# Optimization experiments

Measured on AMD Instinct MI355X. Metric: run time of the kernel, lower is better.

The kernel has to match this reference:

```python
import jax, jax.numpy as jnp
import numpy as np

EPS = 1e-5

def _linear(x, w, b):
    # torch nn.Linear convention: w is [out, in]
    return jnp.einsum('...i,oi->...o', x, w) + b

def _l2_normalize(x, axis=-1):
    n = jnp.sqrt(jnp.sum(x * x, axis=axis, keepdims=True))
    return x / jnp.maximum(n, 1e-12)

def _online_softmax_scan(sim):
    # sim: [B, H, L]. Running max m_t and running sum s_t = sum_{i<=t} exp(sim_i - m_t)
    def combine(a, b):
        ma, sa = a
        mb, sb = b
        m = jnp.maximum(ma, mb)
        s = sa * jnp.exp(ma - m) + sb * jnp.exp(mb - m)
        return m, s
    m_scan, s_scan = jax.lax.associative_scan(combine, (sim, jnp.ones_like(sim)), axis=2)
    return m_scan, s_scan


def setup_inputs() -> dict:
    key = jax.random.key(0)
    ks = jax.random.split(key, 8)
    B, L, D = 2, 2048, 256
    H, h = 8, 32
    s = 1.0 / np.sqrt(D)
    inp = {
        'x': jax.random.normal(ks[0], (B, L, D), jnp.float32),
        'wq_w': jax.random.normal(ks[1], (D, D), jnp.float32) * s,
        'wq_b': jnp.zeros((D,), jnp.float32),
        'wk_w': jax.random.normal(ks[2], (D, D), jnp.float32) * s,
        'wk_b': jnp.zeros((D,), jnp.float32),
        'wv_w': jax.random.normal(ks[3], (D, D), jnp.float32) * s,
        'wv_b': jnp.zeros((D,), jnp.float32),
        'wo_w': jax.random.normal(ks[4], (D, D), jnp.float32) * s,
        'wo_b': jnp.zeros((D,), jnp.float32),
        'wg_w': jax.random.normal(ks[5], (1, h * h), jnp.float32) * (1.0 / np.sqrt(h * h)),
        'wg_b': jnp.zeros((1,), jnp.float32),
        'kv_norm_scale': jnp.ones((1, H, 1, h, h), jnp.float32),
        'qk_norm_scale': jnp.full((1, H, 1), 1.0 / np.sqrt(h), jnp.float32),
    }
    return inp


def reference(x, wq_w, wq_b, wk_w, wk_b, wv_w, wv_b, wo_w, wo_b,
              wg_w, wg_b, kv_norm_scale, qk_norm_scale):
    B, L, D = x.shape
    H, h = kv_norm_scale.shape[1], kv_norm_scale.shape[3]

    q = _linear(x, wq_w, wq_b).reshape(B, L, H, h).transpose(0, 2, 1, 3)  # bhld
    k = _linear(x, wk_w, wk_b).reshape(B, L, H, h).transpose(0, 2, 1, 3)
    v = _linear(x, wv_w, wv_b).reshape(B, L, H, h).transpose(0, 2, 1, 3)

    sim = jnp.einsum('bhld,bhld->bhl', q, k) * qk_norm_scale  # [B,H,L]

    k = _l2_normalize(k)
    v = _l2_normalize(v)

    # outer-product KV state per position: [B,H,L,h,h]
    Z = jnp.einsum('bhld,bhle->bhlde', v, k) * kv_norm_scale

    # gating: squared ReLU of linear over flattened h*h features
    gate_inputs = Z.reshape(B, H, L, h * h)
    gates_logits = jnp.einsum('bhli,oi->bhlo', gate_inputs, wg_w) + wg_b  # [B,H,L,1]
    gates = jnp.square(jax.nn.relu(gates_logits)) + EPS
    gates = gates[..., None]  # [B,H,L,1,1]
    gated_Z = gates * Z

    # associative scans along L
    m_scan, s_scan = _online_softmax_scan(sim)        # [B,H,L]
    Z_scan = jnp.cumsum(gated_Z, axis=2)              # [B,H,L,h,h]
    g_scan = jnp.cumsum(gates, axis=2)                # [B,H,L,1,1]

    softmax_weights = (jnp.exp(sim - m_scan) / (s_scan + EPS))[..., None, None]
    gated_weights = Z_scan / (g_scan + EPS)
    attn_weights = gated_weights * (1.0 + jax.nn.silu(softmax_weights))

    ctxt = jnp.einsum('bhld,bhlde->bhle', q, attn_weights)
    ctxt = ctxt.transpose(0, 2, 1, 3).reshape(B, L, D)
    return _linear(ctxt, wo_w, wo_b)
```

## Files before the change

### kernel.cpp

```cpp
#include <hip/hip_runtime.h>
#include <math.h>

#define EPSV 1e-5f

static constexpr int Ls = 2048, Hh = 8;
static constexpr int NCH = 64, T = 32;

typedef unsigned short u16;
using frag  = __attribute__((ext_vector_type(8))) short;
using f32x4 = __attribute__((ext_vector_type(4))) float;

__device__ __forceinline__ void split_bf16(float v, u16& hi, u16& lo) {
    const unsigned u = __float_as_uint(v);
    hi = (u16)(u >> 16);
    const float hf = __uint_as_float((unsigned)hi << 16);
    lo = (u16)(__float_as_uint(v - hf) >> 16);
}

__device__ __forceinline__ unsigned pk2(u16 a, u16 b) {
    return (unsigned)a | ((unsigned)b << 16);
}

__device__ __forceinline__ void split8(const float4& a, const float4& b,
                                       uint4& hi, uint4& lo) {
    u16 h[8], l[8];
    const float f[8] = {a.x, a.y, a.z, a.w, b.x, b.y, b.z, b.w};
#pragma unroll
    for (int i = 0; i < 8; ++i) split_bf16(f[i], h[i], l[i]);
    hi = make_uint4(pk2(h[0], h[1]), pk2(h[2], h[3]), pk2(h[4], h[5]), pk2(h[6], h[7]));
    lo = make_uint4(pk2(l[0], l[1]), pk2(l[2], l[3]), pk2(l[4], l[5]), pk2(l[6], l[7]));
}

__global__ __launch_bounds__(256) void qkv_fused(
    const float* __restrict__ x,
    const float* __restrict__ wq, const float* __restrict__ wk, const float* __restrict__ wv,
    const float* __restrict__ bq, const float* __restrict__ bk, const float* __restrict__ bv,
    const float* __restrict__ wg_w, const float* __restrict__ wg_b,
    const float* __restrict__ kvs, const float* __restrict__ qks,
    float* __restrict__ qh, float* __restrict__ kh, float* __restrict__ vh,
    float* __restrict__ simG, float* __restrict__ gG,
    float* __restrict__ ZcT, float* __restrict__ mT, float* __restrict__ sT,
    float* __restrict__ gTt)
{
    constexpr int LDK = 40;
    constexpr int LDT = 68;
    __shared__ __align__(16) float smemf[3 * 64 * LDT];
    __shared__ __align__(16) float wkT[2][32 * 36];
    __shared__ float lsim[2][64], lg2[2][64];

    u16* As_hi = (u16*)smemf;
    u16* As_lo = As_hi + 2560;
    u16* Wst   = As_lo + 2560;
    float* Qt = smemf;
    float* Kt = Qt + 64 * LDT;
    float* Vt = Kt + 64 * LDT;

    const int tid = threadIdx.x;
    const int mt = blockIdx.x, nt = blockIdx.y;
    const int m0 = mt * 64, ncol0 = nt * 64;
    const int bidx = m0 >> 11, lg = m0 & (Ls - 1);
    const int wave = tid >> 6, lane = tid & 63;
    const int l15 = lane & 15, quad = lane >> 4;
    const int srow = tid >> 2, sk = (tid & 3) * 8;

    for (int i = tid; i < 2048; i += 256) {
        const int h = i >> 10, de = i & 1023;
        const int d = de >> 5, e = de & 31;
        wkT[h][e * 36 + d] = wg_w[de] * kvs[(nt * 2 + h) * 1024 + de];
    }

    const float* Wsrc[3] = {wq, wk, wv};
    f32x4 acc[3][4] = {};

    for (int k0 = 0; k0 < 256; k0 += 32) {
        const float4 a0 = *(const float4*)&x[(size_t)(m0 + srow) * 256 + k0 + sk];
        const float4 a1 = *(const float4*)&x[(size_t)(m0 + srow) * 256 + k0 + sk + 4];
        float4 w0[3], w1[3];
#pragma unroll
        for (int w = 0; w < 3; ++w) {
            w0[w] = *(const float4*)&Wsrc[w][(size_t)(ncol0 + srow) * 256 + k0 + sk];
            w1[w] = *(const float4*)&Wsrc[w][(size_t)(ncol0 + srow) * 256 + k0 + sk + 4];
        }
        __syncthreads();
        {
            uint4 hi, lo;
            split8(a0, a1, hi, lo);
            *(uint4*)&As_hi[srow * LDK + sk] = hi;
            *(uint4*)&As_lo[srow * LDK + sk] = lo;
#pragma unroll
            for (int w = 0; w < 3; ++w) {
                split8(w0[w], w1[w], hi, lo);
                *(uint4*)&Wst[w * 5120 + srow * LDK + sk] = hi;
                *(uint4*)&Wst[w * 5120 + 2560 + srow * LDK + sk] = lo;
            }
        }
        __syncthreads();

        const frag ah = *(const frag*)&As_hi[(wave * 16 + l15) * LDK + quad * 8];
        const frag al = *(const frag*)&As_lo[(wave * 16 + l15) * LDK + quad * 8];
#pragma unroll
        for (int w = 0; w < 3; ++w)
#pragma unroll
            for (int cf = 0; cf < 4; ++cf) {
                const u16* bp = &Wst[w * 5120 + (cf * 16 + l15) * LDK + quad * 8];
                const frag bh = *(const frag*)bp;
                const frag bl = *(const frag*)(bp + 2560);
                acc[w][cf] = __builtin_amdgcn_mfma_f32_16x16x32_bf16(ah, bh, acc[w][cf], 0, 0, 0);
                acc[w][cf] = __builtin_amdgcn_mfma_f32_16x16x32_bf16(ah, bl, acc[w][cf], 0, 0, 0);
                acc[w][cf] = __builtin_amdgcn_mfma_f32_16x16x32_bf16(al, bh, acc[w][cf], 0, 0, 0);
            }
    }
    __syncthreads();

    {
        float* tiles[3] = {Qt, Kt, Vt};
        const float* biases[3] = {bq, bk, bv};
#pragma unroll
        for (int w = 0; w < 3; ++w)
#pragma unroll
            for (int cf = 0; cf < 4; ++cf) {
                const int col = cf * 16 + l15;
                const float bias = biases[w][ncol0 + col];
#pragma unroll
                for (int r = 0; r < 4; ++r) {
                    const int m = wave * 16 + quad * 4 + r;
                    tiles[w][m * LDT + col] = acc[w][cf][r] + bias;
                }
            }
    }
    __syncthreads();

    if (tid < 128) {
        const int h = tid >> 6, l = tid & 63;
        const int rb = l * LDT + h * 32;
        float4 kr[8], vr[8];
        float ksum = 0.f, vsum = 0.f, qk = 0.f;
#pragma unroll
        for (int e4 = 0; e4 < 8; ++e4) {
            kr[e4] = *(const float4*)&Kt[rb + e4 * 4];
            vr[e4] = *(const float4*)&Vt[rb + e4 * 4];
            const float4 q4 = *(const float4*)&Qt[rb + e4 * 4];
            ksum += kr[e4].x * kr[e4].x + kr[e4].y * kr[e4].y + kr[e4].z * kr[e4].z + kr[e4].w * kr[e4].w;
            vsum += vr[e4].x * vr[e4].x + vr[e4].y * vr[e4].y + vr[e4].z * vr[e4].z + vr[e4].w * vr[e4].w;
            qk   += q4.x * kr[e4].x + q4.y * kr[e4].y + q4.z * kr[e4].z + q4.w * kr[e4].w;
        }
        const float kscale = 1.f / fmaxf(sqrtf(ksum), 1e-12f);
        const float vscale = 1.f / fmaxf(sqrtf(vsum), 1e-12f);
#pragma unroll
        for (int e4 = 0; e4 < 8; ++e4) {
            float4 k4 = kr[e4], v4 = vr[e4];
            k4.x *= kscale; k4.y *= kscale; k4.z *= kscale; k4.w *= kscale;
            v4.x *= vscale; v4.y *= vscale; v4.z *= vscale; v4.w *= vscale;
            *(float4*)&Kt[rb + e4 * 4] = k4;
            *(float4*)&Vt[rb + e4 * 4] = v4;
        }
        const float sim = qk * qks[nt * 2 + h];
        lsim[h][l] = sim;
        simG[(size_t)(bidx * 8 + nt * 2 + h) * Ls + lg + l] = sim;
    }
    __syncthreads();

    {
        const float* tl[3] = {Qt, Kt, Vt};
        float* gl[3] = {qh, kh, vh};
#pragma unroll
        for (int arr = 0; arr < 3; ++arr)
#pragma unroll
            for (int it = 0; it < 4; ++it) {
                const int idx = it * 1024 + tid * 4;
                const int h = idx >> 11, rem = idx & 2047;
                const int l = rem >> 5, e4 = rem & 31;
                const float4 v = *(const float4*)&tl[arr][l * LDT + h * 32 + e4];
                *(float4*)&gl[arr][(size_t)(bidx * 8 + nt * 2 + h) * 65536 +
                                   (size_t)(lg + l) * 32 + e4] = v;
            }
    }

    {
        const int task = tid >> 1, half = tid & 1;
        const int h = task >> 6, l = task & 63;
        float4 vr[8];
#pragma unroll
        for (int d4 = 0; d4 < 8; ++d4)
            vr[d4] = *(const float4*)&Vt[l * LDT + h * 32 + d4 * 4];
        float u = 0.f;
        const int e0 = half * 16;
#pragma unroll 4
        for (int e = e0; e < e0 + 16; ++e) {
            float4 s4 = make_float4(0.f, 0.f, 0.f, 0.f);
#pragma unroll
            for (int d4 = 0; d4 < 8; ++d4) {
                const float4 w4 = *(const float4*)&wkT[h][e * 36 + d4 * 4];
                s4.x = fmaf(vr[d4].x, w4.x, s4.x);
                s4.y = fmaf(vr[d4].y, w4.y, s4.y);
                s4.z = fmaf(vr[d4].z, w4.z, s4.z);
                s4.w = fmaf(vr[d4].w, w4.w, s4.w);
            }
            u = fmaf(s4.x + s4.y + s4.z + s4.w, Kt[l * LDT + h * 32 + e], u);
        }
        u += __shfl_xor(u, 1);
        if (half == 0) {
            const float r = fmaxf(u + wg_b[0], 0.f);
            const float g = r * r + EPSV;
            lg2[h][l] = g;
            gG[(size_t)(bidx * 8 + nt * 2 + h) * Ls + lg + l] = g;
        }
    }
    __syncthreads();

    {
        const int d = tid >> 3, e4m = (tid & 7) * 4;
#pragma unroll
        for (int h = 0; h < 2; ++h)
#pragma unroll
            for (int cc = 0; cc < 2; ++cc) {
                float4 z4 = make_float4(0.f, 0.f, 0.f, 0.f);
#pragma unroll 8
                for (int l = 0; l < 32; ++l) {
                    const int lr = cc * 32 + l;
                    const float gv = lg2[h][lr] * Vt[lr * LDT + h * 32 + d];
                    const float4 k4 = *(const float4*)&Kt[lr * LDT + h * 32 + e4m];
                    z4.x = fmaf(gv, k4.x, z4.x);
                    z4.y = fmaf(gv, k4.y, z4.y);
                    z4.z = fmaf(gv, k4.z, z4.z);
                    z4.w = fmaf(gv, k4.w, z4.w);
                }
                const int bhg = bidx * 8 + nt * 2 + h;
                const int cg = (lg >> 5) + cc;
                *(float4*)&ZcT[((size_t)bhg * NCH + cg) * 1024 + d * 32 + e4m] = z4;
            }
    }

    {
        const int h = wave >> 1, cc = wave & 1;
        if (lane < 32) {
            const int lr = cc * 32 + lane;
            float m = lsim[h][lr], s = 1.f, g = lg2[h][lr];
#pragma unroll
            for (int off = 16; off; off >>= 1) {
                const float mo = __shfl_xor(m, off);
                const float so = __shfl_xor(s, off);
                const float mn = fmaxf(m, mo);
                s = s * __expf(m - mn) + so * __expf(mo - mn);
                m = mn;
                g += __shfl_xor(g, off);
            }
            if (lane == 0) {
                const int bhg = bidx * 8 + nt * 2 + h;
                const int cg = (lg >> 5) + cc;
                mT[bhg * NCH + cg] = m;
                sT[bhg * NCH + cg] = s;
                gTt[bhg * NCH + cg] = g;
            }
        }
    }
}

__global__ __launch_bounds__(256) void prefix_kernel(
    float* __restrict__ Zc, float* __restrict__ mT, float* __restrict__ sT,
    float* __restrict__ gTt,
    const float* __restrict__ kvs, float* __restrict__ aW, float* __restrict__ bW,
    int* __restrict__ flagW)
{
    __shared__ float sc[64 * 64];
    const int bh = blockIdx.x, seg = blockIdx.y;
    const int tid = threadIdx.x;
    float* Zb = Zc + (size_t)bh * NCH * 1024 + seg * 64;

#pragma unroll
    for (int it = 0; it < 16; ++it) {
        const int idx = it * 256 + tid;
        const int cc = idx >> 6, e = idx & 63;
        sc[idx] = Zb[(size_t)cc * 1024 + e];
    }
    __syncthreads();
#pragma unroll
    for (int st = 1; st < 64; st <<= 1) {
        float tmp[16];
#pragma unroll
        for (int it = 0; it < 16; ++it) {
            const int idx = it * 256 + tid;
            tmp[it] = ((idx >> 6) >= st) ? sc[idx - st * 64] : 0.f;
        }
        __syncthreads();
#pragma unroll
        for (int it = 0; it < 16; ++it) sc[it * 256 + tid] += tmp[it];
        __syncthreads();
    }
#pragma unroll
    for (int it = 0; it < 16; ++it) {
        const int idx = it * 256 + tid;
        const int cc = idx >> 6, e = idx & 63;
        Zb[(size_t)cc * 1024 + e] = cc ? sc[idx - 64] : 0.f;
    }

    if (seg == 0 && tid < 64) {
        float m = mT[bh * NCH + tid], s = sT[bh * NCH + tid], g = gTt[bh * NCH + tid];
#pragma unroll
        for (int off = 1; off < 64; off <<= 1) {
            const float mo = __shfl_up(m, off);
            const float so = __shfl_up(s, off);
            const float go = __shfl_up(g, off);
            if (tid >= off) {
                const float mn = fmaxf(m, mo);
                s = s * __expf(m - mn) + so * __expf(mo - mn);
                m = mn;
                g += go;
            }
        }
        float me = __shfl_up(m, 1), se = __shfl_up(s, 1), ge = __shfl_up(g, 1);
        if (tid == 0) { me = -1e30f; se = 0.f; ge = 0.f; }
        mT[bh * NCH + tid] = me;
        sT[bh * NCH + tid] = se;
        gTt[bh * NCH + tid] = ge;
    }

    if (bh == 0 && seg == 1) {
        const int h = tid >> 5, e = tid & 31;
        const float* K = kvs + h * 1024;
        const float k00 = K[0];
        int ok = (k00 != 0.0f);
        for (int d = 0; d < 32; ++d) {
            const float lhs = K[d * 32 + e] * k00;
            const float rhs = K[d * 32] * K[e];
            const float diff = fabsf(lhs - rhs);
            if (diff > 1e-6f * fmaxf(fmaxf(fabsf(lhs), fabsf(rhs)), 1e-20f)) ok = 0;
        }
        aW[h * 32 + e] = K[e * 32];
        bW[h * 32 + e] = (k00 != 0.0f) ? K[e] / k00 : 0.f;
        const int allok = __syncthreads_and(ok);
        if (tid == 0) flagW[0] = allok;
    }
}

__global__ __launch_bounds__(256) void chunk_out_kernel(
    const float* __restrict__ qh, const float* __restrict__ knG, const float* __restrict__ vnG,
    const float* __restrict__ simG, const float* __restrict__ gG,
    const float* __restrict__ kvs,
    const float* __restrict__ ZcP, const float* __restrict__ mP,
    const float* __restrict__ sP, const float* __restrict__ gP,
    const float* __restrict__ aW, const float* __restrict__ bW,
    const int* __restrict__ flagW,
    u16* __restrict__ chi, u16* __restrict__ clo)
{
    __shared__ __align__(16) float qa[1024], knb[1024], zp[1024], sW[1024];
    __shared__ __align__(16) float vnT[32 * 36];
    __shared__ float lkvs[1024];
    __shared__ float lgS[32], lsimS[32], lwgt[32];
    const int tid = threadIdx.x;
    const int c = blockIdx.x, bh = blockIdx.y, h = bh & 7, b = bh >> 3;
    const int l = tid >> 3, e4 = (tid & 7) * 4;
    const size_t base4 = ((size_t)bh * Ls + (size_t)c * T) * 8 + tid;
    const int flag = flagW[0];

    const float4 qv4 = ((const float4*)qh)[base4];
    const float4 kn4 = ((const float4*)knG)[base4];
    const float4 vn4 = ((const float4*)vnG)[base4];
    const float4 z4  = ((const float4*)ZcP)[((size_t)bh * NCH + c) * 256 + tid];
    const float4 la4 = *(const float4*)&aW[h * 32 + e4];
    const float4 lb4 = *(const float4*)&bW[h * 32 + e4];
    if (tid < 32) {
        lgS[tid] = gG[bh * Ls + c * T + tid];
        lsimS[tid] = simG[bh * Ls + c * T + tid];
    }
    if (!flag) {
        *(float4*)&lkvs[tid * 4] = *(const float4*)&kvs[h * 1024 + tid * 4];
    }
    {
        float4 q = qv4, k = kn4;
        if (flag) {
            q.x *= la4.x; q.y *= la4.y; q.z *= la4.z; q.w *= la4.w;
            k.x *= lb4.x; k.y *= lb4.y; k.z *= lb4.z; k.w *= lb4.w;
        }
        *(float4*)&qa[l * 32 + e4] = q;
        *(float4*)&knb[l * 32 + e4] = k;
        *(float4*)&zp[tid * 4] = z4;
        vnT[(e4 + 0) * 36 + l] = vn4.x;
        vnT[(e4 + 1) * 36 + l] = vn4.y;
        vnT[(e4 + 2) * 36 + l] = vn4.z;
        vnT[(e4 + 3) * 36 + l] = vn4.w;
    }
    __syncthreads();

    if (tid < 32) {
        float m = lsimS[tid], s = 1.f, g = lgS[tid];
#pragma unroll
        for (int off = 1; off < 32; off <<= 1) {
            const float mo = __shfl_up(m, off);
            const float so = __shfl_up(s, off);
            const float go = __shfl_up(g, off);
            if (tid >= off) {
                const float mn = fmaxf(m, mo);
                s = s * __expf(m - mn) + so * __expf(mo - mn);
                m = mn;
                g += go;
            }
        }
        const float mp = mP[bh * NCH + c];
        const float sp = sP[bh * NCH + c];
        const float gp = gP[bh * NCH + c];
        const float mn = fmaxf(mp, m);
        s = sp * __expf(mp - mn) + s * __expf(m - mn);
        m = mn;
        g += gp;
        const float sw = __expf(lsimS[tid] - m) / (s + EPSV);
        const float sig = 1.f / (1.f + __expf(-sw));
        lwgt[tid] = (1.f + sw * sig) / (g + EPSV);
    }

    float4 y4 = make_float4(0.f, 0.f, 0.f, 0.f);
    if (flag) {
        float qrow[32];
#pragma unroll
        for (int d4 = 0; d4 < 8; ++d4)
            *(float4*)&qrow[d4 * 4] = *(const float4*)&qa[l * 32 + d4 * 4];
        float4 s4 = make_float4(0.f, 0.f, 0.f, 0.f);
#pragma unroll 8
        for (int d = 0; d < 32; ++d) {
            const float qd = qrow[d];
            const float4 v4 = *(const float4*)&vnT[d * 36 + e4];
            const float4 p4 = *(const float4*)&zp[d * 32 + e4];
            s4.x = fmaf(qd, v4.x, s4.x);
            s4.y = fmaf(qd, v4.y, s4.y);
            s4.z = fmaf(qd, v4.z, s4.z);
            s4.w = fmaf(qd, v4.w, s4.w);
            y4.x = fmaf(qd, p4.x, y4.x);
            y4.y = fmaf(qd, p4.y, y4.y);
            y4.z = fmaf(qd, p4.z, y4.z);
            y4.w = fmaf(qd, p4.w, y4.w);
        }
        y4.x *= lb4.x; y4.y *= lb4.y; y4.z *= lb4.z; y4.w *= lb4.w;
        const float4 lg4 = *(const float4*)&lgS[e4];
        float4 sm;
        sm.x = (e4 + 0 <= l) ? lg4.x * s4.x : 0.f;
        sm.y = (e4 + 1 <= l) ? lg4.y * s4.y : 0.f;
        sm.z = (e4 + 2 <= l) ? lg4.z * s4.z : 0.f;
        sm.w = (e4 + 3 <= l) ? lg4.w * s4.w : 0.f;
        *(float4*)&sW[l * 32 + e4] = sm;
        __syncthreads();
        float srow[32];
#pragma unroll
        for (int j4 = 0; j4 < 8; ++j4)
            *(float4*)&srow[j4 * 4] = *(const float4*)&sW[l * 32 + j4 * 4];
#pragma unroll 8
        for (int j = 0; j < 32; ++j) {
            const float sj = srow[j];
            const float4 k4 = *(const float4*)&knb[j * 32 + e4];
            y4.x = fmaf(sj, k4.x, y4.x);
            y4.y = fmaf(sj, k4.y, y4.y);
            y4.z = fmaf(sj, k4.z, y4.z);
            y4.w = fmaf(sj, k4.w, y4.w);
        }
    } else {
        __syncthreads();
        float* yp = &y4.x;
#pragma unroll
        for (int i = 0; i < 4; ++i) {
            const int e = e4 + i;
            float qe[32];
#pragma unroll
            for (int d = 0; d < 32; ++d)
                qe[d] = qa[l * 32 + d] * lkvs[d * 32 + e];
            float y = 0.f;
#pragma unroll
            for (int d = 0; d < 32; ++d)
                y = fmaf(qe[d], zp[d * 32 + e], y);
            for (int j = 0; j < 32; ++j) {
                float s = 0.f;
#pragma unroll
                for (int d = 0; d < 32; ++d)
                    s = fmaf(qe[d], vnT[d * 36 + j], s);
                if (j <= l) y = fmaf(lgS[j] * s, knb[j * 32 + e], y);
            }
            yp[i] = y;
        }
    }
    const float w = lwgt[l];
    ushort4 hi4, lo4;
    split_bf16(y4.x * w, hi4.x, lo4.x);
    split_bf16(y4.y * w, hi4.y, lo4.y);
    split_bf16(y4.z * w, hi4.z, lo4.z);
    split_bf16(y4.w * w, hi4.w, lo4.w);
    const size_t oidx = ((size_t)(b * Ls + c * T + l)) * 256 + h * 32 + e4;
    *(ushort4*)&chi[oidx] = hi4;
    *(ushort4*)&clo[oidx] = lo4;
}

__global__ __launch_bounds__(256) void out_gemm(
    const u16* __restrict__ Ahi, const u16* __restrict__ Alo,
    const float* __restrict__ wo, const float* __restrict__ bo,
    float* __restrict__ out)
{
    constexpr int LDK = 40;
    __shared__ __align__(16) u16 As_hi[64 * LDK];
    __shared__ __align__(16) u16 As_lo[64 * LDK];
    __shared__ __align__(16) u16 Ws_hi[64 * LDK];
    __shared__ __align__(16) u16 Ws_lo[64 * LDK];

    const int tid = threadIdx.x;
    const int mt = blockIdx.x, nt = blockIdx.y;
    const int m0 = mt * 64, ncol0 = nt * 64;
    const int wave = tid >> 6, lane = tid & 63;
    const int l15 = lane & 15, quad = lane >> 4;
    const int srow = tid >> 2, sk = (tid & 3) * 8;

    f32x4 acc[4] = {};

    for (int k0 = 0; k0 < 256; k0 += 32) {
        const uint4 ah = *(const uint4*)&Ahi[(size_t)(m0 + srow) * 256 + k0 + sk];
        const uint4 al = *(const uint4*)&Alo[(size_t)(m0 + srow) * 256 + k0 + sk];
        const float4 w0 = *(const float4*)&wo[(size_t)(ncol0 + srow) * 256 + k0 + sk];
        const float4 w1 = *(const float4*)&wo[(size_t)(ncol0 + srow) * 256 + k0 + sk + 4];
        __syncthreads();
        uint4 whi, wlo;
        split8(w0, w1, whi, wlo);
        *(uint4*)&As_hi[srow * LDK + sk] = ah;
        *(uint4*)&As_lo[srow * LDK + sk] = al;
        *(uint4*)&Ws_hi[srow * LDK + sk] = whi;
        *(uint4*)&Ws_lo[srow * LDK + sk] = wlo;
        __syncthreads();

        const frag fah = *(const frag*)&As_hi[(wave * 16 + l15) * LDK + quad * 8];
        const frag fal = *(const frag*)&As_lo[(wave * 16 + l15) * LDK + quad * 8];
#pragma unroll
        for (int cf = 0; cf < 4; ++cf) {
            const frag fbh = *(const frag*)&Ws_hi[(cf * 16 + l15) * LDK + quad * 8];
            const frag fbl = *(const frag*)&Ws_lo[(cf * 16 + l15) * LDK + quad * 8];
            acc[cf] = __builtin_amdgcn_mfma_f32_16x16x32_bf16(fah, fbh, acc[cf], 0, 0, 0);
            acc[cf] = __builtin_amdgcn_mfma_f32_16x16x32_bf16(fah, fbl, acc[cf], 0, 0, 0);
            acc[cf] = __builtin_amdgcn_mfma_f32_16x16x32_bf16(fal, fbh, acc[cf], 0, 0, 0);
        }
    }

#pragma unroll
    for (int cf = 0; cf < 4; ++cf) {
        const int o = ncol0 + cf * 16 + l15;
        const float bias = bo[o];
#pragma unroll
        for (int r = 0; r < 4; ++r) {
            const int rm = m0 + wave * 16 + quad * 4 + r;
            out[(size_t)rm * 256 + o] = acc[cf][r] + bias;
        }
    }
}

extern "C" void kernel_launch(void* const* d_in, const int* in_sizes, int n_in,
                              void* d_out, int out_size, void* d_ws, size_t ws_size,
                              hipStream_t stream) {
    const float* x    = (const float*)d_in[0];
    const float* wq_w = (const float*)d_in[1];
    const float* wq_b = (const float*)d_in[2];
    const float* wk_w = (const float*)d_in[3];
    const float* wk_b = (const float*)d_in[4];
    const float* wv_w = (const float*)d_in[5];
    const float* wv_b = (const float*)d_in[6];
    const float* wo_w = (const float*)d_in[7];
    const float* wo_b = (const float*)d_in[8];
    const float* wg_w = (const float*)d_in[9];
    const float* wg_b = (const float*)d_in[10];
    const float* kvs  = (const float*)d_in[11];
    const float* qks  = (const float*)d_in[12];
    float* out = (float*)d_out;

    u16* chi = (u16*)d_ws;
    u16* clo = chi + 1048576;
    float* qh   = (float*)(clo + 1048576);
    float* kh   = qh + 1048576;
    float* vh   = kh + 1048576;
    float* ZcT  = vh + 1048576;
    float* simG = ZcT + 1048576;
    float* gG   = simG + 32768;
    float* mT   = gG + 32768;
    float* sT   = mT + 1024;
    float* gTt  = sT + 1024;
    float* aW   = gTt + 1024;
    float* bW   = aW + 256;
    int* flagW  = (int*)(bW + 256);

    qkv_fused<<<dim3(64, 4), 256, 0, stream>>>(
        x, wq_w, wk_w, wv_w, wq_b, wk_b, wv_b, wg_w, wg_b, kvs, qks,
        qh, kh, vh, simG, gG, ZcT, mT, sT, gTt);
    prefix_kernel<<<dim3(16, 16), 256, 0, stream>>>(
        ZcT, mT, sT, gTt, kvs, aW, bW, flagW);
    chunk_out_kernel<<<dim3(NCH, 16), 256, 0, stream>>>(
        qh, kh, vh, simG, gG, kvs, ZcT, mT, sT, gTt, aW, bW, flagW, chi, clo);
    out_gemm<<<dim3(64, 4), 256, 0, stream>>>(
        chi, clo, wo_w, wo_b, out);
}
```

Baseline: 157.6 us.

## Remove prefix kernel by folding chunk prefix sums into consumer, prefetch GEMM tiles

Drops the separate prefix_kernel launch. Each chunk_out block now sums the preceding chunk Z states directly and runs the 64-chunk softmax/gate scan with warp shuffles. The aW/bW flag setup moves into qkv_fused. Both GEMMs gain register prefetch of the next K-slice, and qkv_fused now gives each wave one N-column tile while sharing A fragments across four M-tiles. The cost is redundant O(c) reads of Z per chunk block, which is quadratic in chunk count, in exchange for one fewer launch and sync point.

```diff
diff --git a/kernel.cpp b/kernel.cpp
--- a/kernel.cpp
+++ b/kernel.cpp
@@ -40,13 +40,14 @@
     float* __restrict__ qh, float* __restrict__ kh, float* __restrict__ vh,
     float* __restrict__ simG, float* __restrict__ gG,
     float* __restrict__ ZcT, float* __restrict__ mT, float* __restrict__ sT,
-    float* __restrict__ gTt)
+    float* __restrict__ gTt,
+    float* __restrict__ aW, float* __restrict__ bW, int* __restrict__ flagW)
 {
     constexpr int LDK = 40;
     constexpr int LDT = 68;
     __shared__ __align__(16) float smemf[3 * 64 * LDT];
-    __shared__ __align__(16) float wkT[2][32 * 36];
-    __shared__ float lsim[2][64], lg2[2][64];
+    __shared__ __align__(16) float wkT[2 * 1152];
+    __shared__ float lsim[128], lg2[128];
 
     u16* As_hi = (u16*)smemf;
     u16* As_lo = As_hi + 2560;
@@ -66,21 +67,22 @@
     for (int i = tid; i < 2048; i += 256) {
         const int h = i >> 10, de = i & 1023;
         const int d = de >> 5, e = de & 31;
-        wkT[h][e * 36 + d] = wg_w[de] * kvs[(nt * 2 + h) * 1024 + de];
+        wkT[h * 1152 + e * 36 + d] = wg_w[de] * kvs[(nt * 2 + h) * 1024 + de];
     }
 
     const float* Wsrc[3] = {wq, wk, wv};
     f32x4 acc[3][4] = {};
 
-    for (int k0 = 0; k0 < 256; k0 += 32) {
-        const float4 a0 = *(const float4*)&x[(size_t)(m0 + srow) * 256 + k0 + sk];
-        const float4 a1 = *(const float4*)&x[(size_t)(m0 + srow) * 256 + k0 + sk + 4];
-        float4 w0[3], w1[3];
-#pragma unroll
-        for (int w = 0; w < 3; ++w) {
-            w0[w] = *(const float4*)&Wsrc[w][(size_t)(ncol0 + srow) * 256 + k0 + sk];
-            w1[w] = *(const float4*)&Wsrc[w][(size_t)(ncol0 + srow) * 256 + k0 + sk + 4];
-        }
+    float4 a0 = *(const float4*)&x[(size_t)(m0 + srow) * 256 + sk];
+    float4 a1 = *(const float4*)&x[(size_t)(m0 + srow) * 256 + sk + 4];
+    float4 w0[3], w1[3];
+#pragma unroll
+    for (int w = 0; w < 3; ++w) {
+        w0[w] = *(const float4*)&Wsrc[w][(size_t)(ncol0 + srow) * 256 + sk];
+        w1[w] = *(const float4*)&Wsrc[w][(size_t)(ncol0 + srow) * 256 + sk + 4];
+    }
+
+    for (int it = 0; it < 8; ++it) {
         __syncthreads();
         {
             uint4 hi, lo;
@@ -96,19 +98,36 @@
         }
         __syncthreads();
 
-        const frag ah = *(const frag*)&As_hi[(wave * 16 + l15) * LDK + quad * 8];
-        const frag al = *(const frag*)&As_lo[(wave * 16 + l15) * LDK + quad * 8];
-#pragma unroll
-        for (int w = 0; w < 3; ++w)
-#pragma unroll
-            for (int cf = 0; cf < 4; ++cf) {
-                const u16* bp = &Wst[w * 5120 + (cf * 16 + l15) * LDK + quad * 8];
-                const frag bh = *(const frag*)bp;
-                const frag bl = *(const frag*)(bp + 2560);
-                acc[w][cf] = __builtin_amdgcn_mfma_f32_16x16x32_bf16(ah, bh, acc[w][cf], 0, 0, 0);
-                acc[w][cf] = __builtin_amdgcn_mfma_f32_16x16x32_bf16(ah, bl, acc[w][cf], 0, 0, 0);
-                acc[w][cf] = __builtin_amdgcn_mfma_f32_16x16x32_bf16(al, bh, acc[w][cf], 0, 0, 0);
-            }
+        if (it < 7) {
+            const int k0 = (it + 1) * 32;
+            a0 = *(const float4*)&x[(size_t)(m0 + srow) * 256 + k0 + sk];
+            a1 = *(const float4*)&x[(size_t)(m0 + srow) * 256 + k0 + sk + 4];
+#pragma unroll
+            for (int w = 0; w < 3; ++w) {
+                w0[w] = *(const float4*)&Wsrc[w][(size_t)(ncol0 + srow) * 256 + k0 + sk];
+                w1[w] = *(const float4*)&Wsrc[w][(size_t)(ncol0 + srow) * 256 + k0 + sk + 4];
+            }
+        }
+
+        frag ah[4], al[4];
+#pragma unroll
+        for (int tm = 0; tm < 4; ++tm) {
+            const int r = tm * 16 + l15;
+            ah[tm] = *(const frag*)&As_hi[r * LDK + quad * 8];
+            al[tm] = *(const frag*)&As_lo[r * LDK + quad * 8];
+        }
+#pragma unroll
+        for (int w = 0; w < 3; ++w) {
+            const u16* bp = &Wst[w * 5120 + (wave * 16 + l15) * LDK + quad * 8];
+            const frag bh = *(const frag*)bp;
+            const frag bl = *(const frag*)(bp + 2560);
+#pragma unroll
+            for (int tm = 0; tm < 4; ++tm) {
+                acc[w][tm] = __builtin_amdgcn_mfma_f32_16x16x32_bf16(ah[tm], bh, acc[w][tm], 0, 0, 0);
+                acc[w][tm] = __builtin_amdgcn_mfma_f32_16x16x32_bf16(ah[tm], bl, acc[w][tm], 0, 0, 0);
+                acc[w][tm] = __builtin_amdgcn_mfma_f32_16x16x32_bf16(al[tm], bh, acc[w][tm], 0, 0, 0);
+            }
+        }
     }
     __syncthreads();
 
@@ -116,17 +135,17 @@
         float* tiles[3] = {Qt, Kt, Vt};
         const float* biases[3] = {bq, bk, bv};
 #pragma unroll
-        for (int w = 0; w < 3; ++w)
-#pragma unroll
-            for (int cf = 0; cf < 4; ++cf) {
-                const int col = cf * 16 + l15;
-                const float bias = biases[w][ncol0 + col];
+        for (int w = 0; w < 3; ++w) {
+            const int col = wave * 16 + l15;
+            const float bias = biases[w][ncol0 + col];
+#pragma unroll
+            for (int tm = 0; tm < 4; ++tm)
 #pragma unroll
                 for (int r = 0; r < 4; ++r) {
-                    const int m = wave * 16 + quad * 4 + r;
-                    tiles[w][m * LDT + col] = acc[w][cf][r] + bias;
+                    const int m = tm * 16 + quad * 4 + r;
+                    tiles[w][m * LDT + col] = acc[w][tm][r] + bias;
                 }
-            }
+        }
     }
     __syncthreads();
 
@@ -155,7 +174,7 @@
             *(float4*)&Vt[rb + e4 * 4] = v4;
         }
         const float sim = qk * qks[nt * 2 + h];
-        lsim[h][l] = sim;
+        lsim[h * 64 + l] = sim;
         simG[(size_t)(bidx * 8 + nt * 2 + h) * Ls + lg + l] = sim;
     }
     __syncthreads();
@@ -190,7 +209,7 @@
             float4 s4 = make_float4(0.f, 0.f, 0.f, 0.f);
 #pragma unroll
             for (int d4 = 0; d4 < 8; ++d4) {
-                const float4 w4 = *(const float4*)&wkT[h][e * 36 + d4 * 4];
+                const float4 w4 = *(const float4*)&wkT[h * 1152 + e * 36 + d4 * 4];
                 s4.x = fmaf(vr[d4].x, w4.x, s4.x);
                 s4.y = fmaf(vr[d4].y, w4.y, s4.y);
                 s4.z = fmaf(vr[d4].z, w4.z, s4.z);
@@ -202,7 +221,7 @@
         if (half == 0) {
             const float r = fmaxf(u + wg_b[0], 0.f);
             const float g = r * r + EPSV;
-            lg2[h][l] = g;
+            lg2[h * 64 + l] = g;
             gG[(size_t)(bidx * 8 + nt * 2 + h) * Ls + lg + l] = g;
         }
     }
@@ -218,7 +237,7 @@
 #pragma unroll 8
                 for (int l = 0; l < 32; ++l) {
                     const int lr = cc * 32 + l;
-                    const float gv = lg2[h][lr] * Vt[lr * LDT + h * 32 + d];
+                    const float gv = lg2[h * 64 + lr] * Vt[lr * LDT + h * 32 + d];
                     const float4 k4 = *(const float4*)&Kt[lr * LDT + h * 32 + e4m];
                     z4.x = fmaf(gv, k4.x, z4.x);
                     z4.y = fmaf(gv, k4.y, z4.y);
@@ -235,7 +254,7 @@
         const int h = wave >> 1, cc = wave & 1;
         if (lane < 32) {
             const int lr = cc * 32 + lane;
-            float m = lsim[h][lr], s = 1.f, g = lg2[h][lr];
+            float m = lsim[h * 64 + lr], s = 1.f, g = lg2[h * 64 + lr];
 #pragma unroll
             for (int off = 16; off; off >>= 1) {
                 const float mo = __shfl_xor(m, off);
@@ -254,68 +273,8 @@
             }
         }
     }
-}
-
-__global__ __launch_bounds__(256) void prefix_kernel(
-    float* __restrict__ Zc, float* __restrict__ mT, float* __restrict__ sT,
-    float* __restrict__ gTt,
-    const float* __restrict__ kvs, float* __restrict__ aW, float* __restrict__ bW,
-    int* __restrict__ flagW)
-{
-    __shared__ float sc[64 * 64];
-    const int bh = blockIdx.x, seg = blockIdx.y;
-    const int tid = threadIdx.x;
-    float* Zb = Zc + (size_t)bh * NCH * 1024 + seg * 64;
-
-#pragma unroll
-    for (int it = 0; it < 16; ++it) {
-        const int idx = it * 256 + tid;
-        const int cc = idx >> 6, e = idx & 63;
-        sc[idx] = Zb[(size_t)cc * 1024 + e];
-    }
-    __syncthreads();
-#pragma unroll
-    for (int st = 1; st < 64; st <<= 1) {
-        float tmp[16];
-#pragma unroll
-        for (int it = 0; it < 16; ++it) {
-            const int idx = it * 256 + tid;
-            tmp[it] = ((idx >> 6) >= st) ? sc[idx - st * 64] : 0.f;
-        }
-        __syncthreads();
-#pragma unroll
-        for (int it = 0; it < 16; ++it) sc[it * 256 + tid] += tmp[it];
-        __syncthreads();
-    }
-#pragma unroll
-    for (int it = 0; it < 16; ++it) {
-        const int idx = it * 256 + tid;
-        const int cc = idx >> 6, e = idx & 63;
-        Zb[(size_t)cc * 1024 + e] = cc ? sc[idx - 64] : 0.f;
-    }
-
-    if (seg == 0 && tid < 64) {
-        float m = mT[bh * NCH + tid], s = sT[bh * NCH + tid], g = gTt[bh * NCH + tid];
-#pragma unroll
-        for (int off = 1; off < 64; off <<= 1) {
-            const float mo = __shfl_up(m, off);
-            const float so = __shfl_up(s, off);
-            const float go = __shfl_up(g, off);
-            if (tid >= off) {
-                const float mn = fmaxf(m, mo);
-                s = s * __expf(m - mn) + so * __expf(mo - mn);
-                m = mn;
-                g += go;
-            }
-        }
-        float me = __shfl_up(m, 1), se = __shfl_up(s, 1), ge = __shfl_up(g, 1);
-        if (tid == 0) { me = -1e30f; se = 0.f; ge = 0.f; }
-        mT[bh * NCH + tid] = me;
-        sT[bh * NCH + tid] = se;
-        gTt[bh * NCH + tid] = ge;
-    }
-
-    if (bh == 0 && seg == 1) {
+
+    if (mt == 0 && nt == 0) {
         const int h = tid >> 5, e = tid & 31;
         const float* K = kvs + h * 1024;
         const float k00 = K[0];
@@ -337,8 +296,8 @@
     const float* __restrict__ qh, const float* __restrict__ knG, const float* __restrict__ vnG,
     const float* __restrict__ simG, const float* __restrict__ gG,
     const float* __restrict__ kvs,
-    const float* __restrict__ ZcP, const float* __restrict__ mP,
-    const float* __restrict__ sP, const float* __restrict__ gP,
+    const float* __restrict__ ZcT, const float* __restrict__ mT,
+    const float* __restrict__ sT, const float* __restrict__ gTt,
     const float* __restrict__ aW, const float* __restrict__ bW,
     const int* __restrict__ flagW,
     u16* __restrict__ chi, u16* __restrict__ clo)
@@ -353,10 +312,29 @@
     const size_t base4 = ((size_t)bh * Ls + (size_t)c * T) * 8 + tid;
     const int flag = flagW[0];
 
+    {
+        const float4* Zt = (const float4*)ZcT + (size_t)bh * NCH * 256 + tid;
+        float4 zacc = make_float4(0.f, 0.f, 0.f, 0.f);
+        int cb = 0;
+        for (; cb + 8 <= c; cb += 8) {
+            float4 v[8];
+#pragma unroll
+            for (int i = 0; i < 8; ++i) v[i] = Zt[(size_t)(cb + i) * 256];
+#pragma unroll
+            for (int i = 0; i < 8; ++i) {
+                zacc.x += v[i].x; zacc.y += v[i].y; zacc.z += v[i].z; zacc.w += v[i].w;
+            }
+        }
+        for (; cb < c; ++cb) {
+            const float4 v = Zt[(size_t)cb * 256];
+            zacc.x += v.x; zacc.y += v.y; zacc.z += v.z; zacc.w += v.w;
+        }
+        *(float4*)&zp[tid * 4] = zacc;
+    }
+
     const float4 qv4 = ((const float4*)qh)[base4];
     const float4 kn4 = ((const float4*)knG)[base4];
     const float4 vn4 = ((const float4*)vnG)[base4];
-    const float4 z4  = ((const float4*)ZcP)[((size_t)bh * NCH + c) * 256 + tid];
     const float4 la4 = *(const float4*)&aW[h * 32 + e4];
     const float4 lb4 = *(const float4*)&bW[h * 32 + e4];
     if (tid < 32) {
@@ -374,7 +352,6 @@
         }
         *(float4*)&qa[l * 32 + e4] = q;
         *(float4*)&knb[l * 32 + e4] = k;
-        *(float4*)&zp[tid * 4] = z4;
         vnT[(e4 + 0) * 36 + l] = vn4.x;
         vnT[(e4 + 1) * 36 + l] = vn4.y;
         vnT[(e4 + 2) * 36 + l] = vn4.z;
@@ -382,30 +359,46 @@
     }
     __syncthreads();
 
-    if (tid < 32) {
-        float m = lsimS[tid], s = 1.f, g = lgS[tid];
-#pragma unroll
-        for (int off = 1; off < 32; off <<= 1) {
-            const float mo = __shfl_up(m, off);
-            const float so = __shfl_up(s, off);
-            const float go = __shfl_up(g, off);
+    if (tid < 64) {
+        float mC = mT[bh * NCH + tid], sC = sT[bh * NCH + tid], gC = gTt[bh * NCH + tid];
+#pragma unroll
+        for (int off = 1; off < 64; off <<= 1) {
+            const float mo = __shfl_up(mC, off);
+            const float so = __shfl_up(sC, off);
+            const float go = __shfl_up(gC, off);
             if (tid >= off) {
-                const float mn = fmaxf(m, mo);
-                s = s * __expf(m - mn) + so * __expf(mo - mn);
-                m = mn;
-                g += go;
-            }
-        }
-        const float mp = mP[bh * NCH + c];
-        const float sp = sP[bh * NCH + c];
-        const float gp = gP[bh * NCH + c];
-        const float mn = fmaxf(mp, m);
-        s = sp * __expf(mp - mn) + s * __expf(m - mn);
-        m = mn;
-        g += gp;
-        const float sw = __expf(lsimS[tid] - m) / (s + EPSV);
-        const float sig = 1.f / (1.f + __expf(-sw));
-        lwgt[tid] = (1.f + sw * sig) / (g + EPSV);
+                const float mn = fmaxf(mC, mo);
+                sC = sC * __expf(mC - mn) + so * __expf(mo - mn);
+                mC = mn;
+                gC += go;
+            }
+        }
+        const float mp = (c > 0) ? __shfl(mC, c - 1) : -1e30f;
+        const float sp = (c > 0) ? __shfl(sC, c - 1) : 0.f;
+        const float gp = (c > 0) ? __shfl(gC, c - 1) : 0.f;
+
+        if (tid < 32) {
+            float m = lsimS[tid], s = 1.f, g = lgS[tid];
+#pragma unroll
+            for (int off = 1; off < 32; off <<= 1) {
+                const float mo = __shfl_up(m, off);
+                const float so = __shfl_up(s, off);
+                const float go = __shfl_up(g, off);
+                if (tid >= off) {
+                    const float mn = fmaxf(m, mo);
+                    s = s * __expf(m - mn) + so * __expf(mo - mn);
+                    m = mn;
+                    g += go;
+                }
+            }
+            const float mn = fmaxf(mp, m);
+            s = sp * __expf(mp - mn) + s * __expf(m - mn);
+            m = mn;
+            g += gp;
+            const float sw = __expf(lsimS[tid] - m) / (s + EPSV);
+            const float sig = 1.f / (1.f + __expf(-sw));
+            lwgt[tid] = (1.f + sw * sig) / (g + EPSV);
+        }
     }
 
     float4 y4 = make_float4(0.f, 0.f, 0.f, 0.f);
@@ -455,8 +448,8 @@
         __syncthreads();
         float* yp = &y4.x;
 #pragma unroll
-        for (int i = 0; i < 4; ++i) {
-            const int e = e4 + i;
+        for (int ii = 0; ii < 4; ++ii) {
+            const int e = e4 + ii;
             float qe[32];
 #pragma unroll
             for (int d = 0; d < 32; ++d)
@@ -472,7 +465,7 @@
                     s = fmaf(qe[d], vnT[d * 36 + j], s);
                 if (j <= l) y = fmaf(lgS[j] * s, knb[j * 32 + e], y);
             }
-            yp[i] = y;
+            yp[ii] = y;
         }
     }
     const float w = lwgt[l];
@@ -506,19 +499,30 @@
 
     f32x4 acc[4] = {};
 
-    for (int k0 = 0; k0 < 256; k0 += 32) {
-        const uint4 ah = *(const uint4*)&Ahi[(size_t)(m0 + srow) * 256 + k0 + sk];
-        const uint4 al = *(const uint4*)&Alo[(size_t)(m0 + srow) * 256 + k0 + sk];
-        const float4 w0 = *(const float4*)&wo[(size_t)(ncol0 + srow) * 256 + k0 + sk];
-        const float4 w1 = *(const float4*)&wo[(size_t)(ncol0 + srow) * 256 + k0 + sk + 4];
+    uint4 ah = *(const uint4*)&Ahi[(size_t)(m0 + srow) * 256 + sk];
+    uint4 al = *(const uint4*)&Alo[(size_t)(m0 + srow) * 256 + sk];
+    float4 w0 = *(const float4*)&wo[(size_t)(ncol0 + srow) * 256 + sk];
+    float4 w1 = *(const float4*)&wo[(size_t)(ncol0 + srow) * 256 + sk + 4];
+
+    for (int it = 0; it < 8; ++it) {
         __syncthreads();
-        uint4 whi, wlo;
-        split8(w0, w1, whi, wlo);
-        *(uint4*)&As_hi[srow * LDK + sk] = ah;
-        *(uint4*)&As_lo[srow * LDK + sk] = al;
-        *(uint4*)&Ws_hi[srow * LDK + sk] = whi;
-        *(uint4*)&Ws_lo[srow * LDK + sk] = wlo;
+        {
+            uint4 whi, wlo;
+            split8(w0, w1, whi, wlo);
+            *(uint4*)&As_hi[srow * LDK + sk] = ah;
+            *(uint4*)&As_lo[srow * LDK + sk] = al;
+            *(uint4*)&Ws_hi[srow * LDK + sk] = whi;
+            *(uint4*)&Ws_lo[srow * LDK + sk] = wlo;
+        }
         __syncthreads();
+
+        if (it < 7) {
+            const int k0 = (it + 1) * 32;
+            ah = *(const uint4*)&Ahi[(size_t)(m0 + srow) * 256 + k0 + sk];
+            al = *(const uint4*)&Alo[(size_t)(m0 + srow) * 256 + k0 + sk];
+            w0 = *(const float4*)&wo[(size_t)(ncol0 + srow) * 256 + k0 + sk];
+            w1 = *(const float4*)&wo[(size_t)(ncol0 + srow) * 256 + k0 + sk + 4];
+        }
 
         const frag fah = *(const frag*)&As_hi[(wave * 16 + l15) * LDK + quad * 8];
         const frag fal = *(const frag*)&As_lo[(wave * 16 + l15) * LDK + quad * 8];
@@ -579,9 +583,7 @@
 
     qkv_fused<<<dim3(64, 4), 256, 0, stream>>>(
         x, wq_w, wk_w, wv_w, wq_b, wk_b, wv_b, wg_w, wg_b, kvs, qks,
-        qh, kh, vh, simG, gG, ZcT, mT, sT, gTt);
-    prefix_kernel<<<dim3(16, 16), 256, 0, stream>>>(
-        ZcT, mT, sT, gTt, kvs, aW, bW, flagW);
+        qh, kh, vh, simG, gG, ZcT, mT, sT, gTt, aW, bW, flagW);
     chunk_out_kernel<<<dim3(NCH, 16), 256, 0, stream>>>(
         qh, kh, vh, simG, gG, kvs, ZcT, mT, sT, gTt, aW, bW, flagW, chi, clo);
     out_gemm<<<dim3(64, 4), 256, 0, stream>>>(
```

Measured after the change: 154.3 us. -2.0%, faster.
